# Kernel tuning notes

Measured on AMD Instinct MI355X. Metric: run time of the kernel, lower is better.

The kernel has to match this reference:

```python
import jax, jax.numpy as jnp
import numpy as np

B = 32
NODES = [20480, 5120, 1280, 320, 80]
K = 6
Z = 64


def _cheb_sparse(x, src, dst, norm, W, b):
    # x: [B, N, F]; Chebyshev recursion with sparse normalized adjacency (edge list)
    def prop(t):
        return jnp.zeros_like(t).at[:, dst, :].add(t[:, src, :] * norm[None, :, None])
    Tx0 = x
    out = jnp.einsum('bnf,fo->bno', Tx0, W[0])
    Tx1 = prop(x)
    out = out + jnp.einsum('bnf,fo->bno', Tx1, W[1])
    for k in range(2, W.shape[0]):
        Tx2 = 2.0 * prop(Tx1) - Tx0
        out = out + jnp.einsum('bnf,fo->bno', Tx2, W[k])
        Tx0, Tx1 = Tx1, Tx2
    return out if b is None else out + b


def _cheb_dense(x, adj, W, b):
    # x: [B, N, F]; adj: dense [N, N] (adjacency_matrices[i].to_dense())
    Tx0 = x
    out = jnp.einsum('bnf,fo->bno', Tx0, W[0])
    Tx1 = jnp.einsum('mn,bnf->bmf', adj, x)
    out = out + jnp.einsum('bnf,fo->bno', Tx1, W[1])
    for k in range(2, W.shape[0]):
        Tx2 = 2.0 * jnp.einsum('mn,bnf->bmf', adj, Tx1) - Tx0
        out = out + jnp.einsum('bnf,fo->bno', Tx2, W[k])
        Tx0, Tx1 = Tx1, Tx2
    return out if b is None else out + b


def _pool(x, idx, w):
    # sparse pooling matrix with <=3 nnz/row: out[b,m,f] = sum_k w[m,k] * x[b, idx[m,k], f]
    return jnp.einsum('mk,bmkf->bmf', w, x[:, idx, :])


def setup_inputs() -> dict:
    key = jax.random.key(0)
    ks = iter(jax.random.split(key, 96))
    N0 = NODES[0]
    E = N0 * 6
    inp = {}
    inp['x'] = jax.random.normal(next(ks), (B * N0, 3), jnp.float32)
    ei = jax.random.randint(next(ks), (2, E), 0, N0, jnp.int32)
    inp['edge_index0'] = ei
    src, dst = ei[0], ei[1]
    deg = jnp.zeros((N0,), jnp.float32).at[src].add(1.0)
    dinv = jnp.where(deg > 0, deg ** -0.5, 0.0)
    inp['A_norm0'] = dinv[src] * dinv[dst]
    inp['batch_size'] = B
    for i in (1, 2, 3):
        n = NODES[i]
        inp[f'adj{i}'] = jax.random.uniform(next(ks), (n, n), jnp.float32) / n
    for i in range(4):
        m, n = NODES[i + 1], NODES[i]
        inp[f'down_idx{i}'] = jax.random.randint(next(ks), (m, 3), 0, n, jnp.int32)
        inp[f'down_w{i}'] = jax.random.uniform(next(ks), (m, 3), jnp.float32) / 3.0
        inp[f'up_idx{i}'] = jax.random.randint(next(ks), (n, 3), 0, m, jnp.int32)
        inp[f'up_w{i}'] = jax.random.uniform(next(ks), (n, 3), jnp.float32) / 3.0
    enc_io = [(3, 16), (16, 16), (16, 16), (16, 32)]
    for i, (fi, fo) in enumerate(enc_io):
        inp[f'W_enc{i}'] = 0.1 * jax.random.normal(next(ks), (K, fi, fo), jnp.float32)
        inp[f'b_enc{i}'] = 0.1 * jax.random.normal(next(ks), (fo,), jnp.float32)
    dec_io = [(32, 16), (16, 16), (16, 16), (16, 16), (16, 3)]
    for i, (fi, fo) in enumerate(dec_io):
        inp[f'W_dec{i}'] = 0.1 * jax.random.normal(next(ks), (K, fi, fo), jnp.float32)
        if i < 4:
            inp[f'b_dec{i}'] = 0.1 * jax.random.normal(next(ks), (fo,), jnp.float32)
    lat_in = NODES[4] * 32  # 2560
    inp['enc_w'] = 0.1 * jax.random.normal(next(ks), (Z, lat_in), jnp.float32)
    inp['enc_b'] = 0.1 * jax.random.normal(next(ks), (Z,), jnp.float32)
    inp['dec_w'] = 0.1 * jax.random.normal(next(ks), (lat_in, Z), jnp.float32)
    inp['dec_b'] = 0.1 * jax.random.normal(next(ks), (lat_in,), jnp.float32)
    return inp


def reference(x, edge_index0, A_norm0, batch_size, adj1, adj2, adj3,
              down_idx0, down_w0, up_idx0, up_w0, down_idx1, down_w1, up_idx1, up_w1,
              down_idx2, down_w2, up_idx2, up_w2, down_idx3, down_w3, up_idx3, up_w3,
              W_enc0, b_enc0, W_enc1, b_enc1, W_enc2, b_enc2, W_enc3, b_enc3,
              W_dec0, b_dec0, W_dec1, b_dec1, W_dec2, b_dec2, W_dec3, b_dec3, W_dec4,
              enc_w, enc_b, dec_w, dec_b):
    relu = jax.nn.relu
    src, dst = edge_index0[0], edge_index0[1]
    h = x.reshape(batch_size, -1, x.shape[-1])
    # encoder
    h = relu(_cheb_sparse(h, src, dst, A_norm0, W_enc0, b_enc0)); h = _pool(h, down_idx0, down_w0)
    h = relu(_cheb_dense(h, adj1, W_enc1, b_enc1)); h = _pool(h, down_idx1, down_w1)
    h = relu(_cheb_dense(h, adj2, W_enc2, b_enc2)); h = _pool(h, down_idx2, down_w2)
    h = relu(_cheb_dense(h, adj3, W_enc3, b_enc3)); h = _pool(h, down_idx3, down_w3)
    z = relu(h.reshape(batch_size, -1) @ enc_w.T + enc_b)
    # decoder
    h = relu(z @ dec_w.T + dec_b).reshape(batch_size, -1, W_dec0.shape[1])
    h = _pool(h, up_idx3, up_w3); h = relu(_cheb_dense(h, adj3, W_dec0, b_dec0))
    h = _pool(h, up_idx2, up_w2); h = relu(_cheb_dense(h, adj2, W_dec1, b_dec1))
    h = _pool(h, up_idx1, up_w1); h = relu(_cheb_dense(h, adj1, W_dec2, b_dec2))
    h = _pool(h, up_idx0, up_w0); h = relu(_cheb_sparse(h, src, dst, A_norm0, W_dec3, b_dec3))
    h = _cheb_sparse(h, src, dst, A_norm0, W_dec4, None)  # final layer, bias=None
    return h.reshape(-1, x.shape[-1])
```

## Files before the change

kernel.cpp:

```cpp
#include <hip/hip_runtime.h>

#define BATCH 32
#define NN0   20480

typedef __attribute__((ext_vector_type(8))) short short8v;
typedef __attribute__((ext_vector_type(4))) float f32x4;

__device__ __forceinline__ float bf2f(unsigned short h) {
    return __uint_as_float(((unsigned int)h) << 16);
}
__device__ __forceinline__ unsigned short f2bf(float x) {
    unsigned int u = __float_as_uint(x);
    u += 0x7fff + ((u >> 16) & 1);
    return (unsigned short)(u >> 16);
}
__device__ __forceinline__ unsigned int pk2(float a, float b) {
    return (unsigned int)f2bf(a) | ((unsigned int)f2bf(b) << 16);
}

__global__ __launch_bounds__(256) void count_kernel(const int* __restrict__ dst, int* __restrict__ cnt, int E) {
    int e = blockIdx.x * 256 + threadIdx.x;
    if (e < E) atomicAdd(&cnt[dst[e]], 1);
}

__global__ __launch_bounds__(256) void scan_kernel(const int* __restrict__ cnt, int* __restrict__ rowptr,
                                                   int* __restrict__ cursor, int n) {
    __shared__ int part[256];
    int tid = threadIdx.x;
    int per = (n + 255) / 256;
    int start = tid * per;
    int end = start + per; if (end > n) end = n; if (start > n) start = n;
    int s = 0;
    for (int i = start; i < end; ++i) s += cnt[i];
    part[tid] = s;
    __syncthreads();
    for (int off = 1; off < 256; off <<= 1) {
        int v = (tid >= off) ? part[tid - off] : 0;
        __syncthreads();
        part[tid] += v;
        __syncthreads();
    }
    int base = (tid == 0) ? 0 : part[tid - 1];
    for (int i = start; i < end; ++i) {
        rowptr[i] = base; cursor[i] = base;
        base += cnt[i];
    }
    if (tid == 255) rowptr[n] = base;
}

__global__ __launch_bounds__(256) void scatter_kernel(const int* __restrict__ src, const int* __restrict__ dst,
                                                      const float* __restrict__ nrm, int* __restrict__ cursor,
                                                      int* __restrict__ esrc, float* __restrict__ ewt,
                                                      int* __restrict__ eid, int E) {
    int e = blockIdx.x * 256 + threadIdx.x;
    if (e >= E) return;
    int p = atomicAdd(&cursor[dst[e]], 1);
    esrc[p] = src[e]; ewt[p] = nrm[e]; eid[p] = e;
}

__global__ __launch_bounds__(256) void sortrows_kernel(const int* __restrict__ rowptr, int* __restrict__ esrc,
                                                       float* __restrict__ ewt, int* __restrict__ eid, int N) {
    int m = blockIdx.x * 256 + threadIdx.x;
    if (m >= N) return;
    int a = rowptr[m], b = rowptr[m + 1];
    for (int i = a + 1; i < b; ++i) {
        int ke = eid[i]; int ks = esrc[i]; float kw = ewt[i];
        int j = i - 1;
        while (j >= a && eid[j] > ke) { eid[j+1]=eid[j]; esrc[j+1]=esrc[j]; ewt[j+1]=ewt[j]; --j; }
        eid[j+1] = ke; esrc[j+1] = ks; ewt[j+1] = kw;
    }
}

__global__ __launch_bounds__(256) void convert_flat(const float* __restrict__ in, unsigned short* __restrict__ out,
                                                    size_t n4) {
    for (size_t i = blockIdx.x * 256 + threadIdx.x; i < n4; i += (size_t)gridDim.x * 256) {
        float4 v = reinterpret_cast<const float4*>(in)[i];
        ushort4 o;
        o.x = f2bf(v.x); o.y = f2bf(v.y); o.z = f2bf(v.z); o.w = f2bf(v.w);
        reinterpret_cast<ushort4*>(out)[i] = o;
    }
}

__global__ __launch_bounds__(256) void xcopy_T(const float* __restrict__ x, unsigned short* __restrict__ out) {
    __shared__ unsigned short sh[32 * 96];
    const int m0 = blockIdx.x * 32;
    const int tid = threadIdx.x;
    const int b = tid >> 3, mi = tid & 7;
#pragma unroll
    for (int ii = 0; ii < 4; ++ii) {
        int mm = mi + ii * 8;
        const float* p = x + ((size_t)b * NN0 + m0 + mm) * 3;
        sh[mm * 96 + b * 3 + 0] = f2bf(p[0]);
        sh[mm * 96 + b * 3 + 1] = f2bf(p[1]);
        sh[mm * 96 + b * 3 + 2] = f2bf(p[2]);
    }
    __syncthreads();
    unsigned int* dst = (unsigned int*)(out + (size_t)m0 * 96);
    const unsigned int* srcp = (const unsigned int*)sh;
    for (int i = tid; i < 32 * 48; i += 256) dst[i] = srcp[i];
}

__global__ __launch_bounds__(256) void sparse_prop16(const int* __restrict__ rowptr, const int* __restrict__ esrc,
                                                     const float* __restrict__ ewt,
                                                     const unsigned short* __restrict__ Tin,
                                                     const unsigned short* __restrict__ Tprev,
                                                     unsigned short* __restrict__ Tout, float s, float t) {
    int g = blockIdx.x * 256 + threadIdx.x;
    int m = g >> 6, lane = g & 63;
    int e0 = rowptr[m], e1 = rowptr[m + 1];
    float acc[8] = {};
    for (int e = e0; e < e1; ++e) {
        float w = ewt[e];
        short8v v = *reinterpret_cast<const short8v*>(Tin + (size_t)esrc[e] * 512 + lane * 8);
#pragma unroll
        for (int j = 0; j < 8; ++j) acc[j] += w * bf2f((unsigned short)v[j]);
    }
    float r[8];
    if (Tprev) {
        short8v pv = *reinterpret_cast<const short8v*>(Tprev + (size_t)m * 512 + lane * 8);
#pragma unroll
        for (int j = 0; j < 8; ++j) r[j] = s * acc[j] + t * bf2f((unsigned short)pv[j]);
    } else {
#pragma unroll
        for (int j = 0; j < 8; ++j) r[j] = s * acc[j];
    }
    uint4 ov;
    ov.x = pk2(r[0], r[1]); ov.y = pk2(r[2], r[3]); ov.z = pk2(r[4], r[5]); ov.w = pk2(r[6], r[7]);
    *reinterpret_cast<uint4*>(Tout + (size_t)m * 512 + lane * 8) = ov;
}

__global__ __launch_bounds__(256) void sparse_prop3(const int* __restrict__ rowptr, const int* __restrict__ esrc,
                                                    const float* __restrict__ ewt,
                                                    const unsigned short* __restrict__ Tin,
                                                    const unsigned short* __restrict__ Tprev,
                                                    unsigned short* __restrict__ Tout, float s, float t) {
    int g = blockIdx.x * 256 + threadIdx.x;
    int m = g / 96, c = g - m * 96;
    int e0 = rowptr[m], e1 = rowptr[m + 1];
    float acc = 0.f;
    for (int e = e0; e < e1; ++e)
        acc += ewt[e] * bf2f(Tin[(size_t)esrc[e] * 96 + c]);
    float v = s * acc;
    if (Tprev) v += t * bf2f(Tprev[(size_t)m * 96 + c]);
    Tout[(size_t)m * 96 + c] = f2bf(v);
}

template <int FIN, int FOUT>
__global__ __launch_bounds__(256) void sparse_epi(const unsigned short* __restrict__ S, size_t slot,
                                                  const float* __restrict__ W, const float* __restrict__ bias,
                                                  unsigned short* __restrict__ out, int relu) {
    __shared__ float Ws[6 * FIN * FOUT];
    for (int i = threadIdx.x; i < 6 * FIN * FOUT; i += 256) Ws[i] = W[i];
    __syncthreads();
    int g = blockIdx.x * 256 + threadIdx.x;
    int m = g >> 5, b = g & 31;
    float oa[FOUT];
#pragma unroll
    for (int o = 0; o < FOUT; ++o) oa[o] = bias ? bias[o] : 0.f;
    for (int k = 0; k < 6; ++k) {
        const unsigned short* p = S + (size_t)k * slot + (size_t)m * (32 * FIN) + b * FIN;
        float xv[FIN];
        if constexpr (FIN == 16) {
            short8v v0 = *reinterpret_cast<const short8v*>(p);
            short8v v1 = *reinterpret_cast<const short8v*>(p + 8);
#pragma unroll
            for (int f = 0; f < 8; ++f) { xv[f] = bf2f((unsigned short)v0[f]); xv[f + 8] = bf2f((unsigned short)v1[f]); }
        } else {
#pragma unroll
            for (int f = 0; f < FIN; ++f) xv[f] = bf2f(p[f]);
        }
#pragma unroll
        for (int f = 0; f < FIN; ++f)
#pragma unroll
            for (int o = 0; o < FOUT; ++o) oa[o] += xv[f] * Ws[(k * FIN + f) * FOUT + o];
    }
    unsigned short* orow = out + (size_t)m * (32 * FOUT) + b * FOUT;
    unsigned int u[FOUT / 2];
#pragma unroll
    for (int o = 0; o < FOUT / 2; ++o) {
        float a = oa[2 * o], c = oa[2 * o + 1];
        if (relu) { a = fmaxf(a, 0.f); c = fmaxf(c, 0.f); }
        u[o] = pk2(a, c);
    }
#pragma unroll
    for (int q = 0; q < FOUT / 8; ++q)
        reinterpret_cast<uint4*>(orow)[q] = make_uint4(u[4 * q], u[4 * q + 1], u[4 * q + 2], u[4 * q + 3]);
}

__global__ __launch_bounds__(256) void sparse_epi_final(const unsigned short* __restrict__ S, size_t slot,
                                                        const float* __restrict__ W, float* __restrict__ dout) {
    __shared__ float Ws[6 * 16 * 3];
    __shared__ float sh[32 * 24];
    for (int i = threadIdx.x; i < 288; i += 256) Ws[i] = W[i];
    __syncthreads();
    const int tid = threadIdx.x;
    const int mm = tid >> 5, b = tid & 31;
    const int m = blockIdx.x * 8 + mm;
    float o0 = 0.f, o1 = 0.f, o2 = 0.f;
    for (int k = 0; k < 6; ++k) {
        const unsigned short* p = S + (size_t)k * slot + (size_t)m * 512 + b * 16;
        short8v v0 = *reinterpret_cast<const short8v*>(p);
        short8v v1 = *reinterpret_cast<const short8v*>(p + 8);
#pragma unroll
        for (int f = 0; f < 16; ++f) {
            float xf = bf2f((unsigned short)(f < 8 ? v0[f] : v1[f - 8]));
            o0 += xf * Ws[(k * 16 + f) * 3 + 0];
            o1 += xf * Ws[(k * 16 + f) * 3 + 1];
            o2 += xf * Ws[(k * 16 + f) * 3 + 2];
        }
    }
    sh[b * 24 + mm * 3 + 0] = o0;
    sh[b * 24 + mm * 3 + 1] = o1;
    sh[b * 24 + mm * 3 + 2] = o2;
    __syncthreads();
    const size_t base = (size_t)blockIdx.x * 24;
    for (int i = tid; i < 768; i += 256) {
        int b2 = i / 24, r = i - b2 * 24;
        dout[(size_t)b2 * (NN0 * 3) + base + r] = sh[i];
    }
}

__device__ __forceinline__ float ldv(const float* p) { return *p; }
__device__ __forceinline__ float ldv(const unsigned short* p) { return bf2f(*p); }

template <typename TI>
__global__ __launch_bounds__(256) void pool_cT(const TI* __restrict__ in, const int* __restrict__ idx,
                                               const float* __restrict__ w, unsigned short* __restrict__ out,
                                               int C, int Mnew) {
    __shared__ float tile[32][33];
    const int m0 = blockIdx.x * 32, c0 = blockIdx.y * 32;
    const int tx = threadIdx.x & 31, ty = threadIdx.x >> 5;
#pragma unroll
    for (int i = 0; i < 4; ++i) {
        int mn = m0 + ty + i * 8;
        const int* ir = idx + mn * 3; const float* wr = w + mn * 3;
        float v = wr[0] * ldv(in + (size_t)ir[0] * C + c0 + tx)
                + wr[1] * ldv(in + (size_t)ir[1] * C + c0 + tx)
                + wr[2] * ldv(in + (size_t)ir[2] * C + c0 + tx);
        tile[ty + i * 8][tx] = v;
    }
    __syncthreads();
#pragma unroll
    for (int i = 0; i < 4; ++i) {
        int c = c0 + ty + i * 8;
        out[(size_t)c * Mnew + m0 + tx] = f2bf(tile[tx][ty + i * 8]);
    }
}

__global__ __launch_bounds__(256) void pool_row16(const unsigned short* __restrict__ in, const int* __restrict__ idx,
                                                  const float* __restrict__ w, unsigned short* __restrict__ out) {
    int g = blockIdx.x * 256 + threadIdx.x;
    int m = g >> 6, lane = g & 63;
    const int* ir = idx + m * 3; const float* wr = w + m * 3;
    short8v a = *reinterpret_cast<const short8v*>(in + (size_t)ir[0] * 512 + lane * 8);
    short8v b = *reinterpret_cast<const short8v*>(in + (size_t)ir[1] * 512 + lane * 8);
    short8v c = *reinterpret_cast<const short8v*>(in + (size_t)ir[2] * 512 + lane * 8);
    float r[8];
#pragma unroll
    for (int j = 0; j < 8; ++j)
        r[j] = wr[0] * bf2f((unsigned short)a[j]) + wr[1] * bf2f((unsigned short)b[j]) + wr[2] * bf2f((unsigned short)c[j]);
    uint4 ov;
    ov.x = pk2(r[0], r[1]); ov.y = pk2(r[2], r[3]); ov.z = pk2(r[4], r[5]); ov.w = pk2(r[6], r[7]);
    *reinterpret_cast<uint4*>(out + (size_t)m * 512 + lane * 8) = ov;
}

__global__ __launch_bounds__(256) void pool_f32(const unsigned short* __restrict__ in, const int* __restrict__ idx,
                                                const float* __restrict__ w, float* __restrict__ out) {
    int g = blockIdx.x * 256 + threadIdx.x;
    int m = g >> 10, c = g & 1023;
    const int* ir = idx + m * 3; const float* wr = w + m * 3;
    out[g] = wr[0] * bf2f(in[(size_t)ir[0] * 1024 + c])
           + wr[1] * bf2f(in[(size_t)ir[1] * 1024 + c])
           + wr[2] * bf2f(in[(size_t)ir[2] * 1024 + c]);
}

template <int MF>
__global__ __launch_bounds__(256) void gemm_mfma(const unsigned short* __restrict__ Ab,
                                                 const unsigned short* __restrict__ Xb,
                                                 const unsigned short* __restrict__ Pb,
                                                 unsigned short* __restrict__ Ob,
                                                 int Mn, float s, float t) {
    constexpr int BM = MF * 64;
    const int K = Mn;
    __shared__ unsigned short As[BM * 64];
    __shared__ unsigned short Xs[64 * 64];
    const int tid = threadIdx.x;
    const int lane = tid & 63, wid = tid >> 6;
    int lin = blockIdx.y * gridDim.x + blockIdx.x;
    int nwg = gridDim.x * gridDim.y;
    int lin2 = (lin & 7) * (nwg >> 3) + (lin >> 3);
    int by = lin2 / gridDim.x, bx = lin2 - by * gridDim.x;
    const int bm = by * BM, bc = bx * 64;

    f32x4 acc[MF][4] = {};
    constexpr int SEGA = (BM * 64 * 2) / 1024 / 4;

    for (int k0 = 0; k0 < K; k0 += 64) {
        __syncthreads();
#pragma unroll
        for (int i = 0; i < SEGA; ++i) {
            int o = (wid * SEGA + i) * 1024 + lane * 16;
            int row = o >> 7;
            int colb = (o & 127) ^ ((row & 7) << 4);
            const unsigned short* g = Ab + (size_t)(bm + row) * K + k0 + (colb >> 1);
            __builtin_amdgcn_global_load_lds((const __attribute__((address_space(1))) void*)g,
                                             (__attribute__((address_space(3))) void*)((char*)As + (size_t)(wid * SEGA + i) * 1024),
                                             16, 0, 0);
        }
#pragma unroll
        for (int i = 0; i < 2; ++i) {
            int o = (wid * 2 + i) * 1024 + lane * 16;
            int row = o >> 7;
            int colb = (o & 127) ^ ((row & 7) << 4);
            const unsigned short* g = Xb + (size_t)(bc + row) * K + k0 + (colb >> 1);
            __builtin_amdgcn_global_load_lds((const __attribute__((address_space(1))) void*)g,
                                             (__attribute__((address_space(3))) void*)((char*)Xs + (size_t)(wid * 2 + i) * 1024),
                                             16, 0, 0);
        }
        __syncthreads();
#pragma unroll
        for (int kk = 0; kk < 2; ++kk) {
            short8v a[MF], b[4];
#pragma unroll
            for (int mf = 0; mf < MF; ++mf) {
                int r = wid * (MF * 16) + mf * 16 + (lane & 15);
                int cb = kk * 64 + ((lane >> 4) * 16);
                int addr = r * 128 + (cb ^ ((r & 7) << 4));
                a[mf] = *reinterpret_cast<const short8v*>((const char*)As + addr);
            }
#pragma unroll
            for (int cf = 0; cf < 4; ++cf) {
                int r = cf * 16 + (lane & 15);
                int cb = kk * 64 + ((lane >> 4) * 16);
                int addr = r * 128 + (cb ^ ((r & 7) << 4));
                b[cf] = *reinterpret_cast<const short8v*>((const char*)Xs + addr);
            }
#pragma unroll
            for (int mf = 0; mf < MF; ++mf)
#pragma unroll
                for (int cf = 0; cf < 4; ++cf)
                    acc[mf][cf] = __builtin_amdgcn_mfma_f32_16x16x32_bf16(a[mf], b[cf], acc[mf][cf], 0, 0, 0);
        }
    }
#pragma unroll
    for (int mf = 0; mf < MF; ++mf) {
        int m0 = bm + wid * (MF * 16) + mf * 16 + ((lane >> 4) * 4);
#pragma unroll
        for (int cf = 0; cf < 4; ++cf) {
            int c = bc + cf * 16 + (lane & 15);
            size_t base = (size_t)c * Mn + m0;
            float v0 = s * acc[mf][cf][0], v1 = s * acc[mf][cf][1];
            float v2 = s * acc[mf][cf][2], v3 = s * acc[mf][cf][3];
            if (Pb) {
                uint2 pv = *reinterpret_cast<const uint2*>(Pb + base);
                v0 += t * bf2f((unsigned short)(pv.x & 0xffff));
                v1 += t * bf2f((unsigned short)(pv.x >> 16));
                v2 += t * bf2f((unsigned short)(pv.y & 0xffff));
                v3 += t * bf2f((unsigned short)(pv.y >> 16));
            }
            uint2 ov;
            ov.x = pk2(v0, v1); ov.y = pk2(v2, v3);
            *reinterpret_cast<uint2*>(Ob + base) = ov;
        }
    }
}

template <int FIN, int FOUT>
__global__ __launch_bounds__(256) void epi_layer(const unsigned short* __restrict__ Tb, size_t tslot,
                                                 const float* __restrict__ W, const float* __restrict__ bias,
                                                 unsigned short* __restrict__ out, int M) {
    __shared__ float Ws[6 * FIN * FOUT];
    for (int i = threadIdx.x; i < 6 * FIN * FOUT; i += 256) Ws[i] = W[i];
    __syncthreads();
    int g = blockIdx.x * 256 + threadIdx.x;
    int b = g / M, m = g - b * M;
    float oa[FOUT];
#pragma unroll
    for (int o = 0; o < FOUT; ++o) oa[o] = bias[o];
    for (int k = 0; k < 6; ++k) {
        const unsigned short* Tk = Tb + (size_t)k * tslot + (size_t)b * FIN * M + m;
#pragma unroll
        for (int f = 0; f < FIN; ++f) {
            float xf = bf2f(Tk[(size_t)f * M]);
#pragma unroll
            for (int o = 0; o < FOUT; ++o) oa[o] += xf * Ws[(k * FIN + f) * FOUT + o];
        }
    }
    unsigned short* orow = out + (size_t)m * (32 * FOUT) + b * FOUT;
    unsigned int u[FOUT / 2];
#pragma unroll
    for (int o = 0; o < FOUT / 2; ++o)
        u[o] = pk2(fmaxf(oa[2 * o], 0.f), fmaxf(oa[2 * o + 1], 0.f));
#pragma unroll
    for (int q = 0; q < FOUT / 8; ++q)
        reinterpret_cast<uint4*>(orow)[q] = make_uint4(u[4 * q], u[4 * q + 1], u[4 * q + 2], u[4 * q + 3]);
}

__global__ __launch_bounds__(256) void fc_enc_kernel(const float* __restrict__ h, const float* __restrict__ w,
                                                     const float* __restrict__ bias, float* __restrict__ z) {
    __shared__ float sh[256];
    int b = blockIdx.x, o = threadIdx.x & 63, q = threadIdx.x >> 6;
    float acc = 0.f;
    for (int n = q * 20; n < q * 20 + 20; ++n)
#pragma unroll
        for (int f = 0; f < 32; ++f)
            acc += h[((size_t)n * 32 + b) * 32 + f] * w[(size_t)o * 2560 + n * 32 + f];
    sh[threadIdx.x] = acc;
    __syncthreads();
    if (q == 0) z[b * 64 + o] = fmaxf(sh[o] + sh[64 + o] + sh[128 + o] + sh[192 + o] + bias[o], 0.f);
}

__global__ __launch_bounds__(256) void fc_dec_kernel(const float* __restrict__ z, const float* __restrict__ w,
                                                     const float* __restrict__ bias, float* __restrict__ out) {
    int g = blockIdx.x * 256 + threadIdx.x;
    if (g >= 80 * 32 * 32) return;
    int f = g % 32; int b = (g / 32) % 32; int n = g / 1024;
    int j = n * 32 + f;
    float acc = bias[j];
    const float* wr = w + (size_t)j * 64;
    const float* zr = z + b * 64;
#pragma unroll
    for (int o = 0; o < 64; ++o) acc += zr[o] * wr[o];
    out[g] = fmaxf(acc, 0.f);
}

extern "C" void kernel_launch(void* const* d_in, const int* in_sizes, int n_in,
                              void* d_out, int out_size, void* d_ws, size_t ws_size,
                              hipStream_t stream) {
    (void)n_in; (void)out_size; (void)ws_size;
    const float* x     = (const float*)d_in[0];
    const int*   ei    = (const int*)d_in[1];
    const float* anorm = (const float*)d_in[2];
    const float* adjs[3] = { (const float*)d_in[4], (const float*)d_in[5], (const float*)d_in[6] };
    const int*   dn_idx[4] = { (const int*)d_in[7],  (const int*)d_in[11], (const int*)d_in[15], (const int*)d_in[19] };
    const float* dn_w[4]   = { (const float*)d_in[8],(const float*)d_in[12],(const float*)d_in[16],(const float*)d_in[20] };
    const int*   up_idx[4] = { (const int*)d_in[9],  (const int*)d_in[13], (const int*)d_in[17], (const int*)d_in[21] };
    const float* up_w[4]   = { (const float*)d_in[10],(const float*)d_in[14],(const float*)d_in[18],(const float*)d_in[22] };
    const float* W_enc[4] = { (const float*)d_in[23], (const float*)d_in[25], (const float*)d_in[27], (const float*)d_in[29] };
    const float* b_enc[4] = { (const float*)d_in[24], (const float*)d_in[26], (const float*)d_in[28], (const float*)d_in[30] };
    const float* W_dec[5] = { (const float*)d_in[31], (const float*)d_in[33], (const float*)d_in[35], (const float*)d_in[37], (const float*)d_in[39] };
    const float* b_dec[4] = { (const float*)d_in[32], (const float*)d_in[34], (const float*)d_in[36], (const float*)d_in[38] };
    const float* enc_w = (const float*)d_in[40];
    const float* enc_b = (const float*)d_in[41];
    const float* dec_w = (const float*)d_in[42];
    const float* dec_b = (const float*)d_in[43];
    const int E = in_sizes[2];

    const size_t SLOT16 = (size_t)NN0 * 512;
    const size_t SLOT3  = (size_t)NN0 * 96;
    unsigned short* S = (unsigned short*)d_ws;
    unsigned short* Tb = S + 3 * SLOT16;
    unsigned short* HB = Tb + (size_t)6 * 512 * 5120;
    char* p = (char*)(HB + SLOT16);
    unsigned short* adj1b = (unsigned short*)p; p += (size_t)5120 * 5120 * 2;
    unsigned short* adj2b = (unsigned short*)p; p += (size_t)1280 * 1280 * 2;
    unsigned short* adj3b = (unsigned short*)p; p += (size_t)320 * 320 * 2;
    int* rowptr = (int*)p;  p += (NN0 + 4) * sizeof(int);
    int* cnt    = (int*)p;  p += NN0 * sizeof(int);
    int* cursor = (int*)p;  p += NN0 * sizeof(int);
    int* esrc   = (int*)p;  p += (size_t)E * sizeof(int);
    int* eid    = (int*)p;  p += (size_t)E * sizeof(int);
    float* ewt  = (float*)p; p += (size_t)E * sizeof(float);
    float* lat0 = (float*)p; p += 80 * 1024 * sizeof(float);
    float* zb   = (float*)p; p += 32 * 64 * sizeof(float);
    float* lat1 = (float*)p;

    hipMemsetAsync(cnt, 0, NN0 * sizeof(int), stream);
    count_kernel<<<(E + 255) / 256, 256, 0, stream>>>(ei + E, cnt, E);
    scan_kernel<<<1, 256, 0, stream>>>(cnt, rowptr, cursor, NN0);
    scatter_kernel<<<(E + 255) / 256, 256, 0, stream>>>(ei, ei + E, anorm, cursor, esrc, ewt, eid, E);
    sortrows_kernel<<<(NN0 + 255) / 256, 256, 0, stream>>>(rowptr, esrc, ewt, eid, NN0);

    convert_flat<<<2048, 256, 0, stream>>>(adjs[0], adj1b, (size_t)5120 * 5120 / 4);
    convert_flat<<<512, 256, 0, stream>>>(adjs[1], adj2b, (size_t)1280 * 1280 / 4);
    convert_flat<<<64, 256, 0, stream>>>(adjs[2], adj3b, (size_t)320 * 320 / 4);

    auto dense_layer = [&](const unsigned short* Ab, int M, int FIN, int FOUT,
                           const float* W, const float* bias, unsigned short* HBout) {
        const int C = 32 * FIN;
        const size_t tslot = (size_t)C * M;
        const int BMv = (M == 320) ? 64 : 128;
        dim3 gg(C / 64, M / BMv);
        for (int k = 1; k < 6; ++k) {
            const unsigned short* Xin = Tb + (size_t)(k - 1) * tslot;
            const unsigned short* Pv  = (k >= 2) ? Tb + (size_t)(k - 2) * tslot : nullptr;
            unsigned short* Oo = Tb + (size_t)k * tslot;
            float s = (k == 1) ? 1.f : 2.f;
            float t = (k == 1) ? 0.f : -1.f;
            if (M == 320) gemm_mfma<1><<<gg, 256, 0, stream>>>(Ab, Xin, Pv, Oo, M, s, t);
            else          gemm_mfma<2><<<gg, 256, 0, stream>>>(Ab, Xin, Pv, Oo, M, s, t);
        }
        int blocks = M * 32 / 256;
        if (FIN == 16 && FOUT == 16)      epi_layer<16, 16><<<blocks, 256, 0, stream>>>(Tb, tslot, W, bias, HBout, M);
        else if (FIN == 16 && FOUT == 32) epi_layer<16, 32><<<blocks, 256, 0, stream>>>(Tb, tslot, W, bias, HBout, M);
        else                              epi_layer<32, 16><<<blocks, 256, 0, stream>>>(Tb, tslot, W, bias, HBout, M);
    };
    auto sparse_layer16 = [&](const float* W, const float* bias, int final_relu, unsigned short* out16) {
        for (int k = 1; k < 6; ++k) {
            const unsigned short* Tin = S + (size_t)(k - 1) * SLOT16;
            const unsigned short* Pv  = (k >= 2) ? S + (size_t)(k - 2) * SLOT16 : nullptr;
            sparse_prop16<<<NN0 / 4, 256, 0, stream>>>(rowptr, esrc, ewt, Tin, Pv, S + (size_t)k * SLOT16,
                                                       (k == 1) ? 1.f : 2.f, (k == 1) ? 0.f : -1.f);
        }
        if (out16) sparse_epi<16, 16><<<NN0 * 32 / 256, 256, 0, stream>>>(S, SLOT16, W, bias, out16, final_relu);
        else       sparse_epi_final<<<NN0 / 8, 256, 0, stream>>>(S, SLOT16, W, (float*)d_out);
    };

    xcopy_T<<<NN0 / 32, 256, 0, stream>>>(x, S);
    for (int k = 1; k < 6; ++k) {
        const unsigned short* Tin = S + (size_t)(k - 1) * SLOT3;
        const unsigned short* Pv  = (k >= 2) ? S + (size_t)(k - 2) * SLOT3 : nullptr;
        sparse_prop3<<<NN0 * 96 / 256, 256, 0, stream>>>(rowptr, esrc, ewt, Tin, Pv, S + (size_t)k * SLOT3,
                                                         (k == 1) ? 1.f : 2.f, (k == 1) ? 0.f : -1.f);
    }
    sparse_epi<3, 16><<<NN0 * 32 / 256, 256, 0, stream>>>(S, SLOT3, W_enc[0], b_enc[0], HB, 1);
    { dim3 g(5120 / 32, 512 / 32);  pool_cT<unsigned short><<<g, 256, 0, stream>>>(HB, dn_idx[0], dn_w[0], Tb, 512, 5120); }
    dense_layer(adj1b, 5120, 16, 16, W_enc[1], b_enc[1], HB);
    { dim3 g(1280 / 32, 512 / 32);  pool_cT<unsigned short><<<g, 256, 0, stream>>>(HB, dn_idx[1], dn_w[1], Tb, 512, 1280); }
    dense_layer(adj2b, 1280, 16, 16, W_enc[2], b_enc[2], HB);
    { dim3 g(320 / 32, 512 / 32);   pool_cT<unsigned short><<<g, 256, 0, stream>>>(HB, dn_idx[2], dn_w[2], Tb, 512, 320); }
    dense_layer(adj3b, 320, 16, 32, W_enc[3], b_enc[3], HB);
    pool_f32<<<80 * 1024 / 256, 256, 0, stream>>>(HB, dn_idx[3], dn_w[3], lat0);
    fc_enc_kernel<<<32, 256, 0, stream>>>(lat0, enc_w, enc_b, zb);
    fc_dec_kernel<<<80 * 32 * 32 / 256, 256, 0, stream>>>(zb, dec_w, dec_b, lat1);
    { dim3 g(320 / 32, 1024 / 32);  pool_cT<float><<<g, 256, 0, stream>>>(lat1, up_idx[3], up_w[3], Tb, 1024, 320); }
    dense_layer(adj3b, 320, 32, 16, W_dec[0], b_dec[0], HB);
    { dim3 g(1280 / 32, 512 / 32);  pool_cT<unsigned short><<<g, 256, 0, stream>>>(HB, up_idx[2], up_w[2], Tb, 512, 1280); }
    dense_layer(adj2b, 1280, 16, 16, W_dec[1], b_dec[1], HB);
    { dim3 g(5120 / 32, 512 / 32);  pool_cT<unsigned short><<<g, 256, 0, stream>>>(HB, up_idx[1], up_w[1], Tb, 512, 5120); }
    dense_layer(adj1b, 5120, 16, 16, W_dec[2], b_dec[2], HB);
    pool_row16<<<NN0 / 4, 256, 0, stream>>>(HB, up_idx[0], up_w[0], S);
    sparse_layer16(W_dec[3], b_dec[3], 1, S);
    sparse_layer16(W_dec[4], nullptr, 0, nullptr);
}
```

Before: 1.738 ms.

## Add split-K with separate reduction kernel for dense Chebyshev GEMMs

Splits the K dimension of the dense adjacency GEMMs for the 5120- and 1280-node levels into four chunks along grid z. Each chunk writes fp32 partials into the workspace, and a new reduce kernel sums them and applies the Chebyshev scale and subtraction before writing bf16. This is meant to raise the number of workgroups and improve occupancy on the smaller levels. The cost is extra fp32 partial traffic and an additional launch per step, and the partial buffer aliases the sparse-layer workspace.

```diff
diff --git a/kernel.cpp b/kernel.cpp
--- a/kernel.cpp
+++ b/kernel.cpp
@@ -274,14 +274,14 @@
            + wr[2] * bf2f(in[(size_t)ir[2] * 1024 + c]);
 }
 
-template <int MF>
+template <int MF, bool SPLIT>
 __global__ __launch_bounds__(256) void gemm_mfma(const unsigned short* __restrict__ Ab,
                                                  const unsigned short* __restrict__ Xb,
                                                  const unsigned short* __restrict__ Pb,
                                                  unsigned short* __restrict__ Ob,
-                                                 int Mn, float s, float t) {
+                                                 float* __restrict__ Pf,
+                                                 int Mn, int KC, float s, float t) {
     constexpr int BM = MF * 64;
-    const int K = Mn;
     __shared__ unsigned short As[BM * 64];
     __shared__ unsigned short Xs[64 * 64];
     const int tid = threadIdx.x;
@@ -291,18 +291,19 @@
     int lin2 = (lin & 7) * (nwg >> 3) + (lin >> 3);
     int by = lin2 / gridDim.x, bx = lin2 - by * gridDim.x;
     const int bm = by * BM, bc = bx * 64;
+    const int kbase = SPLIT ? blockIdx.z * KC : 0;
 
     f32x4 acc[MF][4] = {};
     constexpr int SEGA = (BM * 64 * 2) / 1024 / 4;
 
-    for (int k0 = 0; k0 < K; k0 += 64) {
+    for (int k0 = kbase; k0 < kbase + KC; k0 += 64) {
         __syncthreads();
 #pragma unroll
         for (int i = 0; i < SEGA; ++i) {
             int o = (wid * SEGA + i) * 1024 + lane * 16;
             int row = o >> 7;
             int colb = (o & 127) ^ ((row & 7) << 4);
-            const unsigned short* g = Ab + (size_t)(bm + row) * K + k0 + (colb >> 1);
+            const unsigned short* g = Ab + (size_t)(bm + row) * Mn + k0 + (colb >> 1);
             __builtin_amdgcn_global_load_lds((const __attribute__((address_space(1))) void*)g,
                                              (__attribute__((address_space(3))) void*)((char*)As + (size_t)(wid * SEGA + i) * 1024),
                                              16, 0, 0);
@@ -312,7 +313,7 @@
             int o = (wid * 2 + i) * 1024 + lane * 16;
             int row = o >> 7;
             int colb = (o & 127) ^ ((row & 7) << 4);
-            const unsigned short* g = Xb + (size_t)(bc + row) * K + k0 + (colb >> 1);
+            const unsigned short* g = Xb + (size_t)(bc + row) * Mn + k0 + (colb >> 1);
             __builtin_amdgcn_global_load_lds((const __attribute__((address_space(1))) void*)g,
                                              (__attribute__((address_space(3))) void*)((char*)Xs + (size_t)(wid * 2 + i) * 1024),
                                              16, 0, 0);
@@ -349,20 +350,50 @@
         for (int cf = 0; cf < 4; ++cf) {
             int c = bc + cf * 16 + (lane & 15);
             size_t base = (size_t)c * Mn + m0;
-            float v0 = s * acc[mf][cf][0], v1 = s * acc[mf][cf][1];
-            float v2 = s * acc[mf][cf][2], v3 = s * acc[mf][cf][3];
-            if (Pb) {
-                uint2 pv = *reinterpret_cast<const uint2*>(Pb + base);
-                v0 += t * bf2f((unsigned short)(pv.x & 0xffff));
-                v1 += t * bf2f((unsigned short)(pv.x >> 16));
-                v2 += t * bf2f((unsigned short)(pv.y & 0xffff));
-                v3 += t * bf2f((unsigned short)(pv.y >> 16));
+            if constexpr (SPLIT) {
+                size_t zbase = (size_t)blockIdx.z * (size_t)(gridDim.x * 64) * (size_t)Mn;
+                *reinterpret_cast<float4*>(Pf + zbase + base) =
+                    make_float4(acc[mf][cf][0], acc[mf][cf][1], acc[mf][cf][2], acc[mf][cf][3]);
+            } else {
+                float v0 = s * acc[mf][cf][0], v1 = s * acc[mf][cf][1];
+                float v2 = s * acc[mf][cf][2], v3 = s * acc[mf][cf][3];
+                if (Pb) {
+                    uint2 pv = *reinterpret_cast<const uint2*>(Pb + base);
+                    v0 += t * bf2f((unsigned short)(pv.x & 0xffff));
+                    v1 += t * bf2f((unsigned short)(pv.x >> 16));
+                    v2 += t * bf2f((unsigned short)(pv.y & 0xffff));
+                    v3 += t * bf2f((unsigned short)(pv.y >> 16));
+                }
+                uint2 ov;
+                ov.x = pk2(v0, v1); ov.y = pk2(v2, v3);
+                *reinterpret_cast<uint2*>(Ob + base) = ov;
             }
-            uint2 ov;
-            ov.x = pk2(v0, v1); ov.y = pk2(v2, v3);
-            *reinterpret_cast<uint2*>(Ob + base) = ov;
-        }
-    }
+        }
+    }
+}
+
+__global__ __launch_bounds__(256) void sk_reduce(const float* __restrict__ Pf,
+                                                 const unsigned short* __restrict__ Prev,
+                                                 unsigned short* __restrict__ Out,
+                                                 int n4, int KS, float s, float t) {
+    int g = blockIdx.x * 256 + threadIdx.x;
+    if (g >= n4) return;
+    float4 a = reinterpret_cast<const float4*>(Pf)[g];
+    for (int ks = 1; ks < KS; ++ks) {
+        float4 b = reinterpret_cast<const float4*>(Pf)[(size_t)ks * n4 + g];
+        a.x += b.x; a.y += b.y; a.z += b.z; a.w += b.w;
+    }
+    float v0 = s * a.x, v1 = s * a.y, v2 = s * a.z, v3 = s * a.w;
+    if (Prev) {
+        uint2 pv = reinterpret_cast<const uint2*>(Prev)[g];
+        v0 += t * bf2f((unsigned short)(pv.x & 0xffff));
+        v1 += t * bf2f((unsigned short)(pv.x >> 16));
+        v2 += t * bf2f((unsigned short)(pv.y & 0xffff));
+        v3 += t * bf2f((unsigned short)(pv.y >> 16));
+    }
+    uint2 ov;
+    ov.x = pk2(v0, v1); ov.y = pk2(v2, v3);
+    reinterpret_cast<uint2*>(Out)[g] = ov;
 }
 
 template <int FIN, int FOUT>
@@ -449,6 +480,7 @@
     const size_t SLOT16 = (size_t)NN0 * 512;
     const size_t SLOT3  = (size_t)NN0 * 96;
     unsigned short* S = (unsigned short*)d_ws;
+    float* Pf = (float*)d_ws;
     unsigned short* Tb = S + 3 * SLOT16;
     unsigned short* HB = Tb + (size_t)6 * 512 * 5120;
     char* p = (char*)(HB + SLOT16);
@@ -479,16 +511,25 @@
                            const float* W, const float* bias, unsigned short* HBout) {
         const int C = 32 * FIN;
         const size_t tslot = (size_t)C * M;
-        const int BMv = (M == 320) ? 64 : 128;
-        dim3 gg(C / 64, M / BMv);
+        const int CM4 = (int)(tslot / 4);
+        int KS, KC, BMv, MFv;
+        if (M == 5120)      { BMv = 128; MFv = 2; KS = 4; KC = 1280; }
+        else if (M == 1280) { BMv = 64;  MFv = 1; KS = 4; KC = 320;  }
+        else                { BMv = 64;  MFv = 1; KS = 1; KC = M;    }
+        dim3 gg(C / 64, M / BMv, KS);
         for (int k = 1; k < 6; ++k) {
             const unsigned short* Xin = Tb + (size_t)(k - 1) * tslot;
             const unsigned short* Pv  = (k >= 2) ? Tb + (size_t)(k - 2) * tslot : nullptr;
             unsigned short* Oo = Tb + (size_t)k * tslot;
             float s = (k == 1) ? 1.f : 2.f;
             float t = (k == 1) ? 0.f : -1.f;
-            if (M == 320) gemm_mfma<1><<<gg, 256, 0, stream>>>(Ab, Xin, Pv, Oo, M, s, t);
-            else          gemm_mfma<2><<<gg, 256, 0, stream>>>(Ab, Xin, Pv, Oo, M, s, t);
+            if (KS > 1) {
+                if (MFv == 2) gemm_mfma<2, true><<<gg, 256, 0, stream>>>(Ab, Xin, nullptr, nullptr, Pf, M, KC, s, t);
+                else          gemm_mfma<1, true><<<gg, 256, 0, stream>>>(Ab, Xin, nullptr, nullptr, Pf, M, KC, s, t);
+                sk_reduce<<<(CM4 + 255) / 256, 256, 0, stream>>>(Pf, Pv, Oo, CM4, KS, s, t);
+            } else {
+                gemm_mfma<1, false><<<gg, 256, 0, stream>>>(Ab, Xin, Pv, Oo, nullptr, M, KC, s, t);
+            }
         }
         int blocks = M * 32 / 256;
         if (FIN == 16 && FOUT == 16)      epi_layer<16, 16><<<blocks, 256, 0, stream>>>(Tb, tslot, W, bias, HBout, M);
```

Measured after the change: 1.542 ms. 1.13x faster.
